# Optimization experiments

Measured on AMD Instinct MI355X. Metric: run time of the kernel, lower is better.

Reference implementation:

```python
import jax, jax.numpy as jnp
import numpy as np

DEPTH, HEADS, DIM_HEAD = 6, 8, 64
B, N, E = 2, 128, 160
NUM_ATOMS, NF = 100, 127
DIM = NF + 1                 # 128, node feature dim fed to transformer
INNER = HEADS * DIM_HEAD     # 512


def setup_inputs() -> dict:
    key = jax.random.key(0)
    ks = iter(jax.random.split(key, 40))
    f32 = jnp.float32
    def w(shape, scale=0.02):
        return jax.random.normal(next(ks), shape, dtype=f32) * scale
    inp = {
        "indices": jax.random.randint(next(ks), (B, N), 0, NUM_ATOMS),
        "coordinates": jax.random.normal(next(ks), (B, N, 3), dtype=f32),
        "bonds": jax.random.randint(next(ks), (E, 2), 0, N),
        "noise_level": jax.random.uniform(next(ks), (1,), dtype=f32),
        "atom_emb": w((NUM_ATOMS, NF), 1.0),
        "ln1_g": jnp.ones((DEPTH, DIM), f32), "ln1_b": jnp.zeros((DEPTH, DIM), f32),
        "Wq": w((DEPTH, DIM, INNER)), "bq": jnp.zeros((DEPTH, INNER), f32),
        "Wkv": w((DEPTH, DIM, 2 * INNER)), "bkv": jnp.zeros((DEPTH, 2 * INNER), f32),
        "We": w((DEPTH, 3, INNER)), "be": jnp.zeros((DEPTH, INNER), f32),
        "Wo": w((DEPTH, INNER, DIM)), "bo": jnp.zeros((DEPTH, DIM), f32),
        "Wg1": w((DEPTH, 3 * DIM, 1)),
        "ln2_g": jnp.ones((DEPTH, DIM), f32), "ln2_b": jnp.zeros((DEPTH, DIM), f32),
        "W1": w((DEPTH, DIM, 4 * DIM)), "b1": jnp.zeros((DEPTH, 4 * DIM), f32),
        "W2": w((DEPTH, 4 * DIM, DIM)), "b2": jnp.zeros((DEPTH, DIM), f32),
        "Wg2": w((DEPTH, 3 * DIM, 1)),
        "Wlin": w((DIM, 1)), "blin": jnp.zeros((1,), f32),
    }
    return inp


def _ln(x, g, b, eps=1e-5):
    m = jnp.mean(x, -1, keepdims=True)
    v = jnp.mean((x - m) ** 2, -1, keepdims=True)
    return (x - m) * jax.lax.rsqrt(v + eps) * g + b


def _gated_residual(x, res, Wg):
    # gate = sigmoid(Linear([x, res, x-res])); out = x*gate + res*(1-gate)
    gate = jax.nn.sigmoid(jnp.concatenate([x, res, x - res], -1) @ Wg)  # (B,N,1)
    return x * gate + res * (1.0 - gate)


def _forward(indices, bonds, coordinates, noise_level, atom_emb,
             ln1_g, ln1_b, Wq, bq, Wkv, bkv, We, be, Wo, bo, Wg1,
             ln2_g, ln2_b, W1, b1, W2, b2, Wg2, Wlin, blin):
    b, n = indices.shape
    # nodes_embedding: atom embedding + noise-level channel
    noise = jnp.broadcast_to(noise_level.reshape(1, 1, 1).astype(coordinates.dtype), (b, n, 1))
    nodes = jnp.concatenate([atom_emb[indices], noise], -1)  # (B,N,DIM)
    # edges_embedding: vectorized scatter of per-bond coordinate differences
    i, j = bonds[:, 0], bonds[:, 1]
    diff = coordinates[:, i] - coordinates[:, j]             # (B,E,3)
    edges = jnp.zeros((b, n, n, 3), coordinates.dtype)
    edges = edges.at[:, i, j].set(diff).at[:, j, i].set(-diff)

    scale = DIM_HEAD ** -0.5
    for l in range(DEPTH):
        # PreNorm + edge-biased attention (mask is all-ones -> no-op)
        xn = _ln(nodes, ln1_g[l], ln1_b[l])
        q = (xn @ Wq[l] + bq[l]).reshape(b, n, HEADS, DIM_HEAD)
        k, v = jnp.split(xn @ Wkv[l] + bkv[l], 2, -1)
        k = k.reshape(b, n, HEADS, DIM_HEAD)
        v = v.reshape(b, n, HEADS, DIM_HEAD)
        e = (edges @ We[l] + be[l]).reshape(b, n, n, HEADS, DIM_HEAD)
        kk = k[:, None] + e                                   # (B,i,j,H,D)
        vv = v[:, None] + e
        sim = jnp.einsum('bihd,bijhd->bijh', q, kk) * scale
        attn = jax.nn.softmax(sim, axis=2)                    # softmax over j
        out = jnp.einsum('bijh,bijhd->bihd', attn, vv).reshape(b, n, INNER)
        out = out @ Wo[l] + bo[l]
        nodes = _gated_residual(out, nodes, Wg1[l])
        # PreNorm + FeedForward (exact GELU, mult=4) + gated residual
        xn = _ln(nodes, ln2_g[l], ln2_b[l])
        ff = jax.nn.gelu(xn @ W1[l] + b1[l], approximate=False) @ W2[l] + b2[l]
        nodes = _gated_residual(ff, nodes, Wg2[l])
    return jnp.sum(nodes @ Wlin + blin)


def reference(indices, coordinates, bonds, noise_level, atom_emb,
              ln1_g, ln1_b, Wq, bq, Wkv, bkv, We, be, Wo, bo, Wg1,
              ln2_g, ln2_b, W1, b1, W2, b2, Wg2, Wlin, blin):
    return _forward(indices, bonds, coordinates, noise_level, atom_emb,
                    ln1_g, ln1_b, Wq, bq, Wkv, bkv, We, be, Wo, bo, Wg1,
                    ln2_g, ln2_b, W1, b1, W2, b2, Wg2, Wlin, blin)
```

## Files before the change

kernel.cpp:

```cpp
#include <hip/hip_runtime.h>
#include <hip/hip_fp16.h>
#include <math.h>

#define DEPTH 6
#define HEADS 8
#define BB    2
#define NN    128
#define EE    160
#define NF    127
#define DIMM  128
#define INNER 512
#define NNODE 256

typedef _Float16 h2f16 __attribute__((ext_vector_type(2)));

#if defined(__has_builtin)
#if __has_builtin(__builtin_amdgcn_fdot2)
#define HAVE_FDOT2 1
#endif
#endif

__device__ __forceinline__ float fdot2f(h2f16 a, h2f16 b, float c) {
#ifdef HAVE_FDOT2
    return __builtin_amdgcn_fdot2(a, b, c, false);
#else
    return c + (float)a.x * (float)b.x + (float)a.y * (float)b.y;
#endif
}

__device__ __forceinline__ void gload16(const void* g, void* l) {
    __builtin_amdgcn_global_load_lds((const __attribute__((address_space(1))) void*)g,
                                     (__attribute__((address_space(3))) void*)l,
                                     16, 0, 0);
}

template <int N>
__device__ __forceinline__ void wait_vm() {
    __builtin_amdgcn_s_waitcnt((0xF << 8) | (7 << 4) | (N & 0xF) | ((N >> 4) << 14));
}
__device__ __forceinline__ void wait_lgkm0() { __builtin_amdgcn_s_waitcnt(0xC07F); }
__device__ __forceinline__ void sbar0() { __builtin_amdgcn_sched_barrier(0); }

__device__ __forceinline__ void stage8s(const char* gslice, int rowstride,
                                        char* ldsslice, int ln) {
#pragma unroll
    for (int i = 0; i < 8; i++)
        gload16(gslice + (size_t)i * rowstride + ln * 16, ldsslice + i * 1024);
}

__device__ __forceinline__ void fma8h(float4& a0, float4& a1, float s, float4 raw) {
    const __half2* hp = (const __half2*)&raw;
    float2 p0 = __half22float2(hp[0]), p1 = __half22float2(hp[1]);
    float2 p2 = __half22float2(hp[2]), p3 = __half22float2(hp[3]);
    a0.x += s * p0.x; a0.y += s * p0.y; a0.z += s * p1.x; a0.w += s * p1.y;
    a1.x += s * p2.x; a1.y += s * p2.y; a1.z += s * p3.x; a1.w += s * p3.y;
}

__device__ __forceinline__ void gemv512_pipe(const float* act, float* wbuf,
                                             float* s_part,
                                             const char* nextA, const char* nextB,
                                             int nextStride, int w, int ln) {
    float4 a0 = {0,0,0,0}, a1 = {0,0,0,0};
    const float4* w4 = (const float4*)wbuf;
    wait_vm<8>();
#pragma unroll
    for (int r = 0; r < 8; r++)
        fma8h(a0, a1, act[w * 16 + r], w4[r * 64 + ln]);
    wait_lgkm0(); sbar0();
    if (nextA) { stage8s(nextA, nextStride, (char*)wbuf, ln); wait_vm<8>(); }
    else       { wait_vm<0>(); }
#pragma unroll
    for (int r = 8; r < 16; r++)
        fma8h(a0, a1, act[w * 16 + r], w4[r * 64 + ln]);
    wait_lgkm0(); sbar0();
    if (nextB) stage8s(nextB, nextStride, (char*)wbuf + 8192, ln);
    ((float4*)(s_part + w * 512))[ln * 2]     = a0;
    ((float4*)(s_part + w * 512))[ln * 2 + 1] = a1;
}

__device__ __forceinline__ void gemv128_pipe(const float* act, float* wbuf,
                                             float* s_part,
                                             const char* nextA, const char* nextB,
                                             int nextStride, int w, int ln) {
    float2 acc = {0, 0};
    wait_vm<8>();
#pragma unroll 8
    for (int r = 0; r < 32; r++) {
        float raw = wbuf[r * 64 + ln];
        float2 p = __half22float2(*(const __half2*)&raw);
        float a = act[w * 64 + r];
        acc.x += a * p.x; acc.y += a * p.y;
    }
    wait_lgkm0(); sbar0();
    if (nextA) { stage8s(nextA, nextStride, (char*)wbuf, ln); wait_vm<8>(); }
    else       { wait_vm<0>(); }
#pragma unroll 8
    for (int r = 32; r < 64; r++) {
        float raw = wbuf[r * 64 + ln];
        float2 p = __half22float2(*(const __half2*)&raw);
        float a = act[w * 64 + r];
        acc.x += a * p.x; acc.y += a * p.y;
    }
    wait_lgkm0(); sbar0();
    if (nextB) stage8s(nextB, nextStride, (char*)wbuf + 8192, ln);
    s_part[w * 128 + ln * 2]     = acc.x;
    s_part[w * 128 + ln * 2 + 1] = acc.y;
}

template <int N>
__device__ __forceinline__ void block_reduce_n(float* vals, float* sbuf) {
#pragma unroll
    for (int off = 32; off > 0; off >>= 1)
#pragma unroll
        for (int q = 0; q < N; q++) vals[q] += __shfl_xor(vals[q], off, 64);
    int wave = threadIdx.x >> 6;
    if ((threadIdx.x & 63) == 0)
#pragma unroll
        for (int q = 0; q < N; q++) sbuf[wave * N + q] = vals[q];
    __syncthreads();
#pragma unroll
    for (int q = 0; q < N; q++) {
        float r = 0.0f;
#pragma unroll
        for (int g = 0; g < 8; g++) r += sbuf[g * N + q];
        vals[q] = r;
    }
    __syncthreads();
}

__device__ __forceinline__ float gelu_exact(float a) {
    return 0.5f * a * (1.0f + erff(a * 0.70710678f));
}


__global__ __launch_bounds__(512) void k_cvt(const float* Wq, const float* Wkv,
                                             const float* Wo, const float* W1,
                                             const float* W2,
                                             __half* hWq, __half* hWkv, __half* hWo,
                                             __half* hW1, __half* hW2,
                                             const float* blin, float* out) {
    if (blockIdx.x == 0 && threadIdx.x == 0) out[0] = 256.0f * blin[0];
    int g = blockIdx.x * 512 + threadIdx.x;
    const float4* src; __half* dst; int off;
    if (g < 98304)       { src = (const float4*)Wq;  dst = hWq;  off = g; }
    else if (g < 294912) { src = (const float4*)Wkv; dst = hWkv; off = g - 98304; }
    else if (g < 393216) { src = (const float4*)Wo;  dst = hWo;  off = g - 294912; }
    else if (g < 491520) { src = (const float4*)W1;  dst = hW1;  off = g - 393216; }
    else                 { src = (const float4*)W2;  dst = hW2;  off = g - 491520; }
    float4 v = src[off];
    __half2* d2 = (__half2*)(dst + (size_t)off * 4);
    d2[0] = __floats2half2_rn(v.x, v.y);
    d2[1] = __floats2half2_rn(v.z, v.w);
}

__global__ __launch_bounds__(512, 1) void k_pre(const int* indices, const float* noise,
                                                const float* atom_emb,
                                                const float* ln1_g, const float* ln1_b,
                                                const __half* hWq, const float* bq,
                                                const __half* hWkv, const float* bkv,
                                                float* nodes, float* qb,
                                                __half* hk, __half* hv) {
    int bn = blockIdx.x;
    int t  = threadIdx.x;
    int d  = t & 127;
    bool own = (t < 128);
    int w = t >> 6, ln = t & 63;
    __shared__ float arena[32768];
    __shared__ float s_xn[128];
    __shared__ float s_red[48];
    __shared__ float s_part[4096];
    char*  lslice = (char*)arena + w * 16384;
    float* wbuf   = arena + w * 4096;

    const char* WqL  = (const char*)hWq;
    const char* WkvL = (const char*)hWkv;
    stage8s(WqL + w * 16384, 1024, lslice, ln);
    stage8s(WqL + w * 16384 + 8192, 1024, lslice + 8192, ln);

    float nd = 0.0f;
    if (own) {
        int idx = indices[bn];
        nd = (d < NF) ? atom_emb[idx * NF + d] : noise[0];
        nodes[bn * DIMM + d] = nd;
    }
    float vals[2] = {own ? nd : 0.0f, own ? nd * nd : 0.0f};
    block_reduce_n<2>(vals, s_red);
    float m   = vals[0] * (1.0f / 128.0f);
    float var = vals[1] * (1.0f / 128.0f) - m * m;
    if (own) s_xn[d] = (nd - m) * rsqrtf(var + 1e-5f) * ln1_g[d] + ln1_b[d];
    __syncthreads();

    gemv512_pipe(s_xn, wbuf, s_part,
                 WkvL + (size_t)(w * 16) * 2048,
                 WkvL + (size_t)(w * 16 + 8) * 2048, 2048, w, ln);
    __syncthreads();
    {
        float q = bq[t];
#pragma unroll
        for (int g = 0; g < 8; g++) q += s_part[g * 512 + t];
        qb[(size_t)bn * INNER + t] = q;
    }
    __syncthreads();

    gemv512_pipe(s_xn, wbuf, s_part,
                 WkvL + (size_t)(w * 16) * 2048 + 1024,
                 WkvL + (size_t)(w * 16 + 8) * 2048 + 1024, 2048, w, ln);
    __syncthreads();
    {
        float k = bkv[t];
#pragma unroll
        for (int g = 0; g < 8; g++) k += s_part[g * 512 + t];
        hk[(size_t)bn * INNER + t] = __float2half(k);
    }
    __syncthreads();

    gemv512_pipe(s_xn, wbuf, s_part, nullptr, nullptr, 0, w, ln);
    __syncthreads();
    {
        float v = bkv[INNER + t];
#pragma unroll
        for (int g = 0; g < 8; g++) v += s_part[g * 512 + t];
        hv[(size_t)bn * INNER + t] = __float2half(v);
    }
}

__global__ __launch_bounds__(512, 1) void k_layer(int l,
        const float* coords, const int* bonds,
        const float* We, const float* be,
        float* qb, const __half* hkin, const __half* hvin,
        __half* hkout, __half* hvout,
        const __half* hWo, const float* bo, const float* Wg1,
        const float* ln2_g, const float* ln2_b,
        const __half* hW1, const float* b1,
        const __half* hW2, const float* b2,
        const float* Wg2,
        const float* ln1_g, const float* ln1_b,
        const __half* hWq, const float* bq,
        const __half* hWkv, const float* bkv,
        float* nodes, const float* Wlin, float* out) {
    int bn = blockIdx.x;
    int b = bn >> 7, i = bn & 127;
    int t = threadIdx.x;
    int d = t & 127;
    bool own = (t < 128);
    int w = t >> 6, ln = t & 63;

    __shared__ float arena[32768];
    __shared__ float scoord[384];
    __shared__ float sedge[384];
    __shared__ int   sadj[128];
    __shared__ float s_l[64];
    __shared__ float s_ao[512];
    __shared__ float s_h[512];
    __shared__ float s_xn[128];
    __shared__ float s_red[48];
    __shared__ float s_part[4096];
    float* s_o = s_part;
    char*  lslice = (char*)arena + w * 16384;
    float* wbuf   = arena + w * 4096;

    const char* WoL  = (const char*)(hWo + (size_t)l * INNER * DIMM);
    const char* W1L  = (const char*)(hW1 + (size_t)l * DIMM * 4 * DIMM);
    const char* W2L  = (const char*)(hW2 + (size_t)l * 4 * DIMM * DIMM);
    const char* WqL  = (const char*)(hWq + (size_t)(l + 1) * DIMM * INNER);
    const char* WkvL = (const char*)(hWkv + (size_t)(l + 1) * DIMM * 2 * INNER);

    stage8s(WoL + w * 16384, 1024, lslice, ln);
    stage8s(WoL + w * 16384 + 8192, 1024, lslice + 8192, ln);

    const float4* qR4 = (const float4*)(qb + (size_t)bn * INNER);
    const float4* WeR = (const float4*)(We + (size_t)l * 3 * INNER);
    float4 qa  = qR4[ln * 2],        qz  = qR4[ln * 2 + 1];
    float4 w0a = WeR[ln * 2],        w0z = WeR[ln * 2 + 1];
    float4 w1a = WeR[128 + ln * 2],  w1z = WeR[129 + ln * 2];
    float4 w2a = WeR[256 + ln * 2],  w2z = WeR[257 + ln * 2];
    float4 bea = ((const float4*)(be + (size_t)l * INNER))[ln * 2];
    float4 bez = ((const float4*)(be + (size_t)l * INNER))[ln * 2 + 1];
    float res = own ? nodes[bn * DIMM + d] : 0.0f;
    h2f16 qh0 = {(_Float16)qa.x, (_Float16)qa.y};
    h2f16 qh1 = {(_Float16)qa.z, (_Float16)qa.w};
    h2f16 qh2 = {(_Float16)qz.x, (_Float16)qz.y};
    h2f16 qh3 = {(_Float16)qz.z, (_Float16)qz.w};
    float c = qa.x * bea.x + qa.y * bea.y + qa.z * bea.z + qa.w * bea.w
            + qz.x * bez.x + qz.y * bez.y + qz.z * bez.z + qz.w * bez.w;
    c += __shfl_xor(c, 1, 64); c += __shfl_xor(c, 2, 64); c += __shfl_xor(c, 4, 64);

    if (t < 3 * NN) scoord[t] = coords[b * 3 * NN + t];
    if (t < NN) sadj[t] = 0;
    __syncthreads();
    if (t < EE) {
        int e0 = bonds[2 * t], e1 = bonds[2 * t + 1];
        if (e0 == i) sadj[e1] = 1;
        if (e1 == i) sadj[e0] = 1;
    }
    __syncthreads();
    if (t < NN) {
        int j = t;
        float msk = sadj[j] ? 1.0f : 0.0f;
        sedge[3 * j + 0] = msk * (scoord[3 * i + 0] - scoord[3 * j + 0]);
        sedge[3 * j + 1] = msk * (scoord[3 * i + 1] - scoord[3 * j + 1]);
        sedge[3 * j + 2] = msk * (scoord[3 * i + 2] - scoord[3 * j + 2]);
    }
    __syncthreads();

    const float4* kR = (const float4*)(hkin + (size_t)b * NN * INNER);
    const float4* vR = (const float4*)(hvin + (size_t)b * NN * INNER);
    float l_run = 0.0f, S_nb = 0.0f;
    float4 o0 = {0, 0, 0, 0}, o1 = {0, 0, 0, 0};
    int j0 = w * 16;
#pragma unroll
    for (int base = 0; base < 16; base += 4) {
        float4 kraw[4], vraw[4];
#pragma unroll
        for (int p = 0; p < 4; p++) {
            int j = j0 + base + p;
            kraw[p] = kR[j * 64 + ln];
            vraw[p] = vR[j * 64 + ln];
        }
#pragma unroll
        for (int p = 0; p < 4; p++) {
            int j = j0 + base + p;
            const h2f16* kh = (const h2f16*)&kraw[p];
            float s = fdot2f(qh0, kh[0],
                      fdot2f(qh1, kh[1],
                      fdot2f(qh2, kh[2],
                      fdot2f(qh3, kh[3], 0.0f))));
            bool bonded = (sadj[j] != 0);
            float4 e0, e1;
            if (bonded) {
                float ex = sedge[3 * j], ey = sedge[3 * j + 1], ez = sedge[3 * j + 2];
                e0.x = bea.x + ex * w0a.x + ey * w1a.x + ez * w2a.x;
                e0.y = bea.y + ex * w0a.y + ey * w1a.y + ez * w2a.y;
                e0.z = bea.z + ex * w0a.z + ey * w1a.z + ez * w2a.z;
                e0.w = bea.w + ex * w0a.w + ey * w1a.w + ez * w2a.w;
                e1.x = bez.x + ex * w0z.x + ey * w1z.x + ez * w2z.x;
                e1.y = bez.y + ex * w0z.y + ey * w1z.y + ez * w2z.y;
                e1.z = bez.z + ex * w0z.z + ey * w1z.z + ez * w2z.z;
                e1.w = bez.w + ex * w0z.w + ey * w1z.w + ez * w2z.w;
                s += qa.x * e0.x + qa.y * e0.y + qa.z * e0.z + qa.w * e0.w
                   + qz.x * e1.x + qz.y * e1.y + qz.z * e1.z + qz.w * e1.w;
            }
            s += __shfl_xor(s, 1, 64);
            s += __shfl_xor(s, 2, 64);
            s += __shfl_xor(s, 4, 64);
            if (!bonded) s += c;
            float pp = __expf(s * 0.125f);
            l_run += pp;
            const __half2* vh = (const __half2*)&vraw[p];
            float2 v0 = __half22float2(vh[0]), v1 = __half22float2(vh[1]);
            float2 v2 = __half22float2(vh[2]), v3 = __half22float2(vh[3]);
            o0.x += pp * v0.x; o0.y += pp * v0.y; o0.z += pp * v1.x; o0.w += pp * v1.y;
            o1.x += pp * v2.x; o1.y += pp * v2.y; o1.z += pp * v3.x; o1.w += pp * v3.y;
            if (bonded) {
                o0.x += pp * e0.x; o0.y += pp * e0.y; o0.z += pp * e0.z; o0.w += pp * e0.w;
                o1.x += pp * e1.x; o1.y += pp * e1.y; o1.z += pp * e1.z; o1.w += pp * e1.w;
            } else S_nb += pp;
        }
    }
    o0.x += S_nb * bea.x; o0.y += S_nb * bea.y; o0.z += S_nb * bea.z; o0.w += S_nb * bea.w;
    o1.x += S_nb * bez.x; o1.y += S_nb * bez.y; o1.z += S_nb * bez.z; o1.w += S_nb * bez.w;
    ((float4*)(s_o + w * 512))[ln * 2]     = o0;
    ((float4*)(s_o + w * 512))[ln * 2 + 1] = o1;
    if ((ln & 7) == 0) s_l[w * 8 + (ln >> 3)] = l_run;
    __syncthreads();
    {
        float o = 0.0f;
#pragma unroll
        for (int g = 0; g < 8; g++) o += s_o[g * 512 + t];
        int h = t >> 6;
        float lsum = 0.0f;
#pragma unroll
        for (int g = 0; g < 8; g++) lsum += s_l[g * 8 + h];
        s_ao[t] = o / lsum;
    }
    __syncthreads();

    gemv128_pipe(s_ao, wbuf, s_part,
                 W1L + w * 16384, W1L + w * 16384 + 8192, 1024, w, ln);
    __syncthreads();
    float x = 0.0f;
    if (own) {
        x = bo[l * DIMM + d];
#pragma unroll
        for (int g = 0; g < 8; g++) x += s_part[g * 128 + d];
    }

    const float* Wg1_l = Wg1 + l * 3 * DIMM;
    float n1;
    {
        float tex = own ? (x * Wg1_l[d] + res * Wg1_l[DIMM + d]
                           + (x - res) * Wg1_l[2 * DIMM + d]) : 0.0f;
        float vals[6] = {tex,
                         own ? x : 0.0f, own ? x * x : 0.0f,
                         own ? x * res : 0.0f,
                         own ? res : 0.0f, own ? res * res : 0.0f};
        block_reduce_n<6>(vals, s_red);
        float g1 = 1.0f / (1.0f + __expf(-vals[0]));
        float sn  = g1 * vals[1] + (1.0f - g1) * vals[4];
        float sn2 = g1 * g1 * vals[2] + 2.0f * g1 * (1.0f - g1) * vals[3]
                  + (1.0f - g1) * (1.0f - g1) * vals[5];
        float m   = sn * (1.0f / 128.0f);
        float var = sn2 * (1.0f / 128.0f) - m * m;
        n1 = x * g1 + res * (1.0f - g1);
        if (own) s_xn[d] = (n1 - m) * rsqrtf(var + 1e-5f) * ln2_g[l * DIMM + d]
                         + ln2_b[l * DIMM + d];
    }
    __syncthreads();

    gemv512_pipe(s_xn, wbuf, s_part,
                 W2L + w * 16384, W2L + w * 16384 + 8192, 1024, w, ln);
    __syncthreads();
    {
        float a = b1[l * 4 * DIMM + t];
#pragma unroll
        for (int g = 0; g < 8; g++) a += s_part[g * 512 + t];
        s_h[t] = gelu_exact(a);
    }
    __syncthreads();

    gemv128_pipe(s_h, wbuf, s_part,
                 (l < DEPTH - 1) ? WqL + w * 16384 : nullptr,
                 (l < DEPTH - 1) ? WqL + w * 16384 + 8192 : nullptr, 1024, w, ln);
    __syncthreads();
    float y = 0.0f;
    if (own) {
        y = b2[l * DIMM + d];
#pragma unroll
        for (int g = 0; g < 8; g++) y += s_part[g * 128 + d];
    }

    const float* Wg2_l = Wg2 + l * 3 * DIMM;
    if (l < DEPTH - 1) {
        float tex = own ? (y * Wg2_l[d] + n1 * Wg2_l[DIMM + d]
                           + (y - n1) * Wg2_l[2 * DIMM + d]) : 0.0f;
        float vals[6] = {tex,
                         own ? y : 0.0f, own ? y * y : 0.0f,
                         own ? y * n1 : 0.0f,
                         own ? n1 : 0.0f, own ? n1 * n1 : 0.0f};
        block_reduce_n<6>(vals, s_red);
        float g2 = 1.0f / (1.0f + __expf(-vals[0]));
        float sn  = g2 * vals[1] + (1.0f - g2) * vals[4];
        float sn2 = g2 * g2 * vals[2] + 2.0f * g2 * (1.0f - g2) * vals[3]
                  + (1.0f - g2) * (1.0f - g2) * vals[5];
        float m   = sn * (1.0f / 128.0f);
        float var = sn2 * (1.0f / 128.0f) - m * m;
        float n2 = y * g2 + n1 * (1.0f - g2);
        if (own) {
            nodes[bn * DIMM + d] = n2;
            s_xn[d] = (n2 - m) * rsqrtf(var + 1e-5f) * ln1_g[(l + 1) * DIMM + d]
                    + ln1_b[(l + 1) * DIMM + d];
        }
        __syncthreads();

        gemv512_pipe(s_xn, wbuf, s_part,
                     WkvL + (size_t)(w * 16) * 2048,
                     WkvL + (size_t)(w * 16 + 8) * 2048, 2048, w, ln);
        __syncthreads();
        {
            float q = bq[(l + 1) * INNER + t];
#pragma unroll
            for (int g = 0; g < 8; g++) q += s_part[g * 512 + t];
            qb[(size_t)bn * INNER + t] = q;
        }
        __syncthreads();

        gemv512_pipe(s_xn, wbuf, s_part,
                     WkvL + (size_t)(w * 16) * 2048 + 1024,
                     WkvL + (size_t)(w * 16 + 8) * 2048 + 1024, 2048, w, ln);
        __syncthreads();
        {
            float k = bkv[(l + 1) * 2 * INNER + t];
#pragma unroll
            for (int g = 0; g < 8; g++) k += s_part[g * 512 + t];
            hkout[(size_t)bn * INNER + t] = __float2half(k);
        }
        __syncthreads();

        gemv512_pipe(s_xn, wbuf, s_part, nullptr, nullptr, 0, w, ln);
        __syncthreads();
        {
            float v = bkv[(l + 1) * 2 * INNER + INNER + t];
#pragma unroll
            for (int g = 0; g < 8; g++) v += s_part[g * 512 + t];
            hvout[(size_t)bn * INNER + t] = __float2half(v);
        }
    } else {
        float wl = own ? Wlin[d] : 0.0f;
        float tex = own ? (y * Wg2_l[d] + n1 * Wg2_l[DIMM + d]
                           + (y - n1) * Wg2_l[2 * DIMM + d]) : 0.0f;
        float vals[3] = {tex, y * wl, n1 * wl};
        block_reduce_n<3>(vals, s_red);
        float g2 = 1.0f / (1.0f + __expf(-vals[0]));
        float tot = g2 * vals[1] + (1.0f - g2) * vals[2];
        if (t == 0) atomicAdd(out, tot);
    }
}

extern "C" void kernel_launch(void* const* d_in, const int* in_sizes, int n_in,
                              void* d_out, int out_size, void* d_ws, size_t ws_size,
                              hipStream_t stream) {
    const int*   indices = (const int*)d_in[0];
    const float* coords  = (const float*)d_in[1];
    const int*   bonds   = (const int*)d_in[2];
    const float* noise   = (const float*)d_in[3];
    const float* atom_emb= (const float*)d_in[4];
    const float* ln1_g   = (const float*)d_in[5];
    const float* ln1_b   = (const float*)d_in[6];
    const float* Wq      = (const float*)d_in[7];
    const float* bq      = (const float*)d_in[8];
    const float* Wkv     = (const float*)d_in[9];
    const float* bkv     = (const float*)d_in[10];
    const float* We      = (const float*)d_in[11];
    const float* be      = (const float*)d_in[12];
    const float* Wo      = (const float*)d_in[13];
    const float* bo      = (const float*)d_in[14];
    const float* Wg1     = (const float*)d_in[15];
    const float* ln2_g   = (const float*)d_in[16];
    const float* ln2_b   = (const float*)d_in[17];
    const float* W1      = (const float*)d_in[18];
    const float* b1      = (const float*)d_in[19];
    const float* W2      = (const float*)d_in[20];
    const float* b2      = (const float*)d_in[21];
    const float* Wg2     = (const float*)d_in[22];
    const float* Wlin    = (const float*)d_in[23];
    const float* blin    = (const float*)d_in[24];

    float*  ws    = (float*)d_ws;
    float*  nodes = ws;
    float*  qb    = nodes + NNODE * DIMM;
    __half* hkb   = (__half*)(qb + NNODE * INNER);
    __half* hvb   = hkb + 2 * NNODE * INNER;
    __half* hWq   = hvb + 2 * NNODE * INNER;
    __half* hWkv  = hWq + DEPTH * DIMM * INNER;
    __half* hWo   = hWkv + DEPTH * DIMM * 2 * INNER;
    __half* hW1   = hWo + DEPTH * INNER * DIMM;
    __half* hW2   = hW1 + DEPTH * DIMM * 4 * DIMM;

    k_cvt<<<1152, 512, 0, stream>>>(Wq, Wkv, Wo, W1, W2, hWq, hWkv, hWo, hW1, hW2,
                                    blin, (float*)d_out);
    k_pre<<<NNODE, 512, 0, stream>>>(indices, noise, atom_emb, ln1_g, ln1_b,
                                     hWq, bq, hWkv, bkv, nodes, qb, hkb, hvb);
    for (int l = 0; l < DEPTH; l++) {
        const __half* hkin = hkb + (size_t)(l & 1) * NNODE * INNER;
        const __half* hvin = hvb + (size_t)(l & 1) * NNODE * INNER;
        __half* hkout = hkb + (size_t)((l + 1) & 1) * NNODE * INNER;
        __half* hvout = hvb + (size_t)((l + 1) & 1) * NNODE * INNER;
        k_layer<<<NNODE, 512, 0, stream>>>(l, coords, bonds, We, be,
                                           qb, hkin, hvin, hkout, hvout,
                                           hWo, bo, Wg1, ln2_g, ln2_b, hW1, b1, hW2, b2,
                                           Wg2, ln1_g, ln1_b, hWq, bq, hWkv, bkv,
                                           nodes, Wlin, (float*)d_out);
    }
}
```

Measured before the change: 259.6 us.

## Double block size to 1024 threads and re-split GEMV and attention work

Launches k_pre and k_layer with 1024 threads (16 waves) instead of 512. Each wave now handles half the rows of the attention key range and half the column range of every GEMV, with new staging helpers that load half-width weight slices. Partial sums are reduced across 16 waves, and the attention output reduction runs in two passes through shared memory. The aim is more latency hiding and memory parallelism per block, at the cost of extra barriers, a larger reduction and higher register pressure under the 1024-thread launch bound.

```diff
diff --git a/kernel.cpp b/kernel.cpp
--- a/kernel.cpp
+++ b/kernel.cpp
@@ -41,68 +41,81 @@
 __device__ __forceinline__ void wait_lgkm0() { __builtin_amdgcn_s_waitcnt(0xC07F); }
 __device__ __forceinline__ void sbar0() { __builtin_amdgcn_sched_barrier(0); }
 
-__device__ __forceinline__ void stage8s(const char* gslice, int rowstride,
-                                        char* ldsslice, int ln) {
-#pragma unroll
-    for (int i = 0; i < 8; i++)
-        gload16(gslice + (size_t)i * rowstride + ln * 16, ldsslice + i * 1024);
-}
-
-__device__ __forceinline__ void fma8h(float4& a0, float4& a1, float s, float4 raw) {
-    const __half2* hp = (const __half2*)&raw;
-    float2 p0 = __half22float2(hp[0]), p1 = __half22float2(hp[1]);
-    float2 p2 = __half22float2(hp[2]), p3 = __half22float2(hp[3]);
-    a0.x += s * p0.x; a0.y += s * p0.y; a0.z += s * p1.x; a0.w += s * p1.y;
-    a1.x += s * p2.x; a1.y += s * p2.y; a1.z += s * p3.x; a1.w += s * p3.y;
-}
-
-__device__ __forceinline__ void gemv512_pipe(const float* act, float* wbuf,
-                                             float* s_part,
-                                             const char* nextA, const char* nextB,
-                                             int nextStride, int w, int ln) {
-    float4 a0 = {0,0,0,0}, a1 = {0,0,0,0};
-    const float4* w4 = (const float4*)wbuf;
-    wait_vm<8>();
-#pragma unroll
-    for (int r = 0; r < 8; r++)
-        fma8h(a0, a1, act[w * 16 + r], w4[r * 64 + ln]);
+__device__ __forceinline__ void stage4c(const char* g, char* lds, int ln) {
+#pragma unroll
+    for (int i = 0; i < 4; i++)
+        gload16(g + i * 1024 + ln * 16, lds + i * 1024);
+}
+__device__ __forceinline__ void stage4h(const char* g, int rs, char* lds, int ln) {
+#pragma unroll
+    for (int i = 0; i < 4; i++)
+        gload16(g + (size_t)(2 * i + (ln >> 5)) * rs + (ln & 31) * 16, lds + i * 1024);
+}
+
+
+template <int NK>
+__device__ __forceinline__ void gemv512x(const float* act, float* wbuf,
+                                         float* s_part, int w, int ln,
+                                         const char* nextA, const char* nextB,
+                                         int nextRS) {
+    int kg = w >> 1;
+    float4 acc = {0, 0, 0, 0};
+    const float2* w2 = (const float2*)wbuf;
+    wait_vm<4>();
+#pragma unroll
+    for (int r = 0; r < 8; r++) {
+        float2 raw = w2[r * 64 + ln];
+        const __half2* hp = (const __half2*)&raw;
+        float2 p0 = __half22float2(hp[0]), p1 = __half22float2(hp[1]);
+        float a = act[kg * 16 + r];
+        acc.x += a * p0.x; acc.y += a * p0.y; acc.z += a * p1.x; acc.w += a * p1.y;
+    }
     wait_lgkm0(); sbar0();
-    if (nextA) { stage8s(nextA, nextStride, (char*)wbuf, ln); wait_vm<8>(); }
-    else       { wait_vm<0>(); }
-#pragma unroll
-    for (int r = 8; r < 16; r++)
-        fma8h(a0, a1, act[w * 16 + r], w4[r * 64 + ln]);
+    if (NK == 1)      { stage4c(nextA, (char*)wbuf, ln);         wait_vm<4>(); }
+    else if (NK == 2) { stage4h(nextA, nextRS, (char*)wbuf, ln); wait_vm<4>(); }
+    else              { wait_vm<0>(); }
+#pragma unroll
+    for (int r = 8; r < 16; r++) {
+        float2 raw = w2[r * 64 + ln];
+        const __half2* hp = (const __half2*)&raw;
+        float2 p0 = __half22float2(hp[0]), p1 = __half22float2(hp[1]);
+        float a = act[kg * 16 + r];
+        acc.x += a * p0.x; acc.y += a * p0.y; acc.z += a * p1.x; acc.w += a * p1.y;
+    }
     wait_lgkm0(); sbar0();
-    if (nextB) stage8s(nextB, nextStride, (char*)wbuf + 8192, ln);
-    ((float4*)(s_part + w * 512))[ln * 2]     = a0;
-    ((float4*)(s_part + w * 512))[ln * 2 + 1] = a1;
-}
-
-__device__ __forceinline__ void gemv128_pipe(const float* act, float* wbuf,
-                                             float* s_part,
-                                             const char* nextA, const char* nextB,
-                                             int nextStride, int w, int ln) {
+    if (NK == 1)      stage4c(nextB, (char*)wbuf + 4096, ln);
+    else if (NK == 2) stage4h(nextB, nextRS, (char*)wbuf + 4096, ln);
+    ((float4*)(s_part + w * 256))[ln] = acc;
+}
+
+template <int NK>
+__device__ __forceinline__ void gemv128x(const float* act, float* wbuf,
+                                         float* s_part, int w, int ln,
+                                         const char* nextA, const char* nextB,
+                                         int nextRS) {
     float2 acc = {0, 0};
-    wait_vm<8>();
+    wait_vm<4>();
 #pragma unroll 8
-    for (int r = 0; r < 32; r++) {
+    for (int r = 0; r < 16; r++) {
         float raw = wbuf[r * 64 + ln];
         float2 p = __half22float2(*(const __half2*)&raw);
-        float a = act[w * 64 + r];
+        float a = act[w * 32 + r];
         acc.x += a * p.x; acc.y += a * p.y;
     }
     wait_lgkm0(); sbar0();
-    if (nextA) { stage8s(nextA, nextStride, (char*)wbuf, ln); wait_vm<8>(); }
-    else       { wait_vm<0>(); }
+    if (NK == 1)      { stage4c(nextA, (char*)wbuf, ln);         wait_vm<4>(); }
+    else if (NK == 2) { stage4h(nextA, nextRS, (char*)wbuf, ln); wait_vm<4>(); }
+    else              { wait_vm<0>(); }
 #pragma unroll 8
-    for (int r = 32; r < 64; r++) {
+    for (int r = 16; r < 32; r++) {
         float raw = wbuf[r * 64 + ln];
         float2 p = __half22float2(*(const __half2*)&raw);
-        float a = act[w * 64 + r];
+        float a = act[w * 32 + r];
         acc.x += a * p.x; acc.y += a * p.y;
     }
     wait_lgkm0(); sbar0();
-    if (nextB) stage8s(nextB, nextStride, (char*)wbuf + 8192, ln);
+    if (NK == 1)      stage4c(nextB, (char*)wbuf + 4096, ln);
+    else if (NK == 2) stage4h(nextB, nextRS, (char*)wbuf + 4096, ln);
     s_part[w * 128 + ln * 2]     = acc.x;
     s_part[w * 128 + ln * 2 + 1] = acc.y;
 }
@@ -122,7 +135,7 @@
     for (int q = 0; q < N; q++) {
         float r = 0.0f;
 #pragma unroll
-        for (int g = 0; g < 8; g++) r += sbuf[g * N + q];
+        for (int g = 0; g < 16; g++) r += sbuf[g * N + q];
         vals[q] = r;
     }
     __syncthreads();
@@ -153,29 +166,30 @@
     d2[1] = __floats2half2_rn(v.z, v.w);
 }
 
-__global__ __launch_bounds__(512, 1) void k_pre(const int* indices, const float* noise,
-                                                const float* atom_emb,
-                                                const float* ln1_g, const float* ln1_b,
-                                                const __half* hWq, const float* bq,
-                                                const __half* hWkv, const float* bkv,
-                                                float* nodes, float* qb,
-                                                __half* hk, __half* hv) {
+__global__ __launch_bounds__(1024, 4) void k_pre(const int* indices, const float* noise,
+                                                 const float* atom_emb,
+                                                 const float* ln1_g, const float* ln1_b,
+                                                 const __half* hWq, const float* bq,
+                                                 const __half* hWkv, const float* bkv,
+                                                 float* nodes, float* qb,
+                                                 __half* hk, __half* hv) {
     int bn = blockIdx.x;
     int t  = threadIdx.x;
     int d  = t & 127;
     bool own = (t < 128);
     int w = t >> 6, ln = t & 63;
+    int kg = w >> 1, ch = w & 1;
     __shared__ float arena[32768];
     __shared__ float s_xn[128];
-    __shared__ float s_red[48];
+    __shared__ float s_red[96];
     __shared__ float s_part[4096];
-    char*  lslice = (char*)arena + w * 16384;
-    float* wbuf   = arena + w * 4096;
+    float* wbuf = arena + w * 2048;
 
     const char* WqL  = (const char*)hWq;
     const char* WkvL = (const char*)hWkv;
-    stage8s(WqL + w * 16384, 1024, lslice, ln);
-    stage8s(WqL + w * 16384 + 8192, 1024, lslice + 8192, ln);
+
+    stage4h(WqL + (size_t)(kg * 16) * 1024 + ch * 512, 1024, (char*)wbuf, ln);
+    stage4h(WqL + (size_t)(kg * 16 + 8) * 1024 + ch * 512, 1024, (char*)wbuf + 4096, ln);
 
     float nd = 0.0f;
     if (own) {
@@ -190,41 +204,44 @@
     if (own) s_xn[d] = (nd - m) * rsqrtf(var + 1e-5f) * ln1_g[d] + ln1_b[d];
     __syncthreads();
 
-    gemv512_pipe(s_xn, wbuf, s_part,
-                 WkvL + (size_t)(w * 16) * 2048,
-                 WkvL + (size_t)(w * 16 + 8) * 2048, 2048, w, ln);
-    __syncthreads();
-    {
+    gemv512x<2>(s_xn, wbuf, s_part, w, ln,
+                WkvL + (size_t)(kg * 16) * 2048 + ch * 512,
+                WkvL + (size_t)(kg * 16 + 8) * 2048 + ch * 512, 2048);
+    __syncthreads();
+    if (t < 512) {
+        int lc = t & 255, cch = t >> 8;
         float q = bq[t];
 #pragma unroll
-        for (int g = 0; g < 8; g++) q += s_part[g * 512 + t];
+        for (int g = 0; g < 8; g++) q += s_part[(g * 2 + cch) * 256 + lc];
         qb[(size_t)bn * INNER + t] = q;
     }
     __syncthreads();
 
-    gemv512_pipe(s_xn, wbuf, s_part,
-                 WkvL + (size_t)(w * 16) * 2048 + 1024,
-                 WkvL + (size_t)(w * 16 + 8) * 2048 + 1024, 2048, w, ln);
-    __syncthreads();
-    {
+    gemv512x<2>(s_xn, wbuf, s_part, w, ln,
+                WkvL + (size_t)(kg * 16) * 2048 + 1024 + ch * 512,
+                WkvL + (size_t)(kg * 16 + 8) * 2048 + 1024 + ch * 512, 2048);
+    __syncthreads();
+    if (t < 512) {
+        int lc = t & 255, cch = t >> 8;
         float k = bkv[t];
 #pragma unroll
-        for (int g = 0; g < 8; g++) k += s_part[g * 512 + t];
+        for (int g = 0; g < 8; g++) k += s_part[(g * 2 + cch) * 256 + lc];
         hk[(size_t)bn * INNER + t] = __float2half(k);
     }
     __syncthreads();
 
-    gemv512_pipe(s_xn, wbuf, s_part, nullptr, nullptr, 0, w, ln);
-    __syncthreads();
-    {
+    gemv512x<0>(s_xn, wbuf, s_part, w, ln, nullptr, nullptr, 0);
+    __syncthreads();
+    if (t < 512) {
+        int lc = t & 255, cch = t >> 8;
         float v = bkv[INNER + t];
 #pragma unroll
-        for (int g = 0; g < 8; g++) v += s_part[g * 512 + t];
+        for (int g = 0; g < 8; g++) v += s_part[(g * 2 + cch) * 256 + lc];
         hv[(size_t)bn * INNER + t] = __float2half(v);
     }
 }
 
-__global__ __launch_bounds__(512, 1) void k_layer(int l,
+__global__ __launch_bounds__(1024, 4) void k_layer(int l,
         const float* coords, const int* bonds,
         const float* We, const float* be,
         float* qb, const __half* hkin, const __half* hvin,
@@ -244,20 +261,19 @@
     int d = t & 127;
     bool own = (t < 128);
     int w = t >> 6, ln = t & 63;
+    int kg = w >> 1, ch = w & 1;
 
     __shared__ float arena[32768];
     __shared__ float scoord[384];
     __shared__ float sedge[384];
     __shared__ int   sadj[128];
-    __shared__ float s_l[64];
+    __shared__ float s_l[128];
     __shared__ float s_ao[512];
     __shared__ float s_h[512];
     __shared__ float s_xn[128];
-    __shared__ float s_red[48];
+    __shared__ float s_red[96];
     __shared__ float s_part[4096];
-    float* s_o = s_part;
-    char*  lslice = (char*)arena + w * 16384;
-    float* wbuf   = arena + w * 4096;
+    float* wbuf = arena + w * 2048;
 
     const char* WoL  = (const char*)(hWo + (size_t)l * INNER * DIMM);
     const char* W1L  = (const char*)(hW1 + (size_t)l * DIMM * 4 * DIMM);
@@ -265,8 +281,8 @@
     const char* WqL  = (const char*)(hWq + (size_t)(l + 1) * DIMM * INNER);
     const char* WkvL = (const char*)(hWkv + (size_t)(l + 1) * DIMM * 2 * INNER);
 
-    stage8s(WoL + w * 16384, 1024, lslice, ln);
-    stage8s(WoL + w * 16384 + 8192, 1024, lslice + 8192, ln);
+    stage4c(WoL + w * 8192, (char*)wbuf, ln);
+    stage4c(WoL + w * 8192 + 4096, (char*)wbuf + 4096, ln);
 
     const float4* qR4 = (const float4*)(qb + (size_t)bn * INNER);
     const float4* WeR = (const float4*)(We + (size_t)l * 3 * INNER);
@@ -307,9 +323,9 @@
     const float4* vR = (const float4*)(hvin + (size_t)b * NN * INNER);
     float l_run = 0.0f, S_nb = 0.0f;
     float4 o0 = {0, 0, 0, 0}, o1 = {0, 0, 0, 0};
-    int j0 = w * 16;
-#pragma unroll
-    for (int base = 0; base < 16; base += 4) {
+    int j0 = w * 8;
+#pragma unroll
+    for (int base = 0; base < 8; base += 4) {
         float4 kraw[4], vraw[4];
 #pragma unroll
         for (int p = 0; p < 4; p++) {
@@ -359,30 +375,44 @@
     }
     o0.x += S_nb * bea.x; o0.y += S_nb * bea.y; o0.z += S_nb * bea.z; o0.w += S_nb * bea.w;
     o1.x += S_nb * bez.x; o1.y += S_nb * bez.y; o1.z += S_nb * bez.z; o1.w += S_nb * bez.w;
-    ((float4*)(s_o + w * 512))[ln * 2]     = o0;
-    ((float4*)(s_o + w * 512))[ln * 2 + 1] = o1;
     if ((ln & 7) == 0) s_l[w * 8 + (ln >> 3)] = l_run;
-    __syncthreads();
-    {
-        float o = 0.0f;
-#pragma unroll
-        for (int g = 0; g < 8; g++) o += s_o[g * 512 + t];
+
+    if (w < 8) {
+        ((float4*)(s_part + w * 512))[ln * 2]     = o0;
+        ((float4*)(s_part + w * 512))[ln * 2 + 1] = o1;
+    }
+    __syncthreads();
+    float oacc = 0.0f;
+    if (t < 512) {
+#pragma unroll
+        for (int g = 0; g < 8; g++) oacc += s_part[g * 512 + t];
+    }
+    __syncthreads();
+    if (w >= 8) {
+        ((float4*)(s_part + (w - 8) * 512))[ln * 2]     = o0;
+        ((float4*)(s_part + (w - 8) * 512))[ln * 2 + 1] = o1;
+    }
+    __syncthreads();
+    if (t < 512) {
+#pragma unroll
+        for (int g = 0; g < 8; g++) oacc += s_part[g * 512 + t];
         int h = t >> 6;
         float lsum = 0.0f;
 #pragma unroll
-        for (int g = 0; g < 8; g++) lsum += s_l[g * 8 + h];
-        s_ao[t] = o / lsum;
-    }
-    __syncthreads();
-
-    gemv128_pipe(s_ao, wbuf, s_part,
-                 W1L + w * 16384, W1L + w * 16384 + 8192, 1024, w, ln);
+        for (int g = 0; g < 16; g++) lsum += s_l[g * 8 + h];
+        s_ao[t] = oacc / lsum;
+    }
+    __syncthreads();
+
+    gemv128x<2>(s_ao, wbuf, s_part, w, ln,
+                W1L + (size_t)(kg * 16) * 1024 + ch * 512,
+                W1L + (size_t)(kg * 16 + 8) * 1024 + ch * 512, 1024);
     __syncthreads();
     float x = 0.0f;
     if (own) {
         x = bo[l * DIMM + d];
 #pragma unroll
-        for (int g = 0; g < 8; g++) x += s_part[g * 128 + d];
+        for (int g = 0; g < 16; g++) x += s_part[g * 128 + d];
     }
 
     const float* Wg1_l = Wg1 + l * 3 * DIMM;
@@ -407,26 +437,30 @@
     }
     __syncthreads();
 
-    gemv512_pipe(s_xn, wbuf, s_part,
-                 W2L + w * 16384, W2L + w * 16384 + 8192, 1024, w, ln);
-    __syncthreads();
-    {
+    gemv512x<1>(s_xn, wbuf, s_part, w, ln,
+                W2L + w * 8192, W2L + w * 8192 + 4096, 0);
+    __syncthreads();
+    if (t < 512) {
+        int lc = t & 255, cch = t >> 8;
         float a = b1[l * 4 * DIMM + t];
 #pragma unroll
-        for (int g = 0; g < 8; g++) a += s_part[g * 512 + t];
+        for (int g = 0; g < 8; g++) a += s_part[(g * 2 + cch) * 256 + lc];
         s_h[t] = gelu_exact(a);
     }
     __syncthreads();
 
-    gemv128_pipe(s_h, wbuf, s_part,
-                 (l < DEPTH - 1) ? WqL + w * 16384 : nullptr,
-                 (l < DEPTH - 1) ? WqL + w * 16384 + 8192 : nullptr, 1024, w, ln);
+    if (l < DEPTH - 1)
+        gemv128x<2>(s_h, wbuf, s_part, w, ln,
+                    WqL + (size_t)(kg * 16) * 1024 + ch * 512,
+                    WqL + (size_t)(kg * 16 + 8) * 1024 + ch * 512, 1024);
+    else
+        gemv128x<0>(s_h, wbuf, s_part, w, ln, nullptr, nullptr, 0);
     __syncthreads();
     float y = 0.0f;
     if (own) {
         y = b2[l * DIMM + d];
 #pragma unroll
-        for (int g = 0; g < 8; g++) y += s_part[g * 128 + d];
+        for (int g = 0; g < 16; g++) y += s_part[g * 128 + d];
     }
 
     const float* Wg2_l = Wg2 + l * 3 * DIMM;
@@ -452,36 +486,39 @@
         }
         __syncthreads();
 
-        gemv512_pipe(s_xn, wbuf, s_part,
-                     WkvL + (size_t)(w * 16) * 2048,
-                     WkvL + (size_t)(w * 16 + 8) * 2048, 2048, w, ln);
+        gemv512x<2>(s_xn, wbuf, s_part, w, ln,
+                    WkvL + (size_t)(kg * 16) * 2048 + ch * 512,
+                    WkvL + (size_t)(kg * 16 + 8) * 2048 + ch * 512, 2048);
         __syncthreads();
-        {
+        if (t < 512) {
+            int lc = t & 255, cch = t >> 8;
             float q = bq[(l + 1) * INNER + t];
 #pragma unroll
-            for (int g = 0; g < 8; g++) q += s_part[g * 512 + t];
+            for (int g = 0; g < 8; g++) q += s_part[(g * 2 + cch) * 256 + lc];
             qb[(size_t)bn * INNER + t] = q;
         }
         __syncthreads();
 
-        gemv512_pipe(s_xn, wbuf, s_part,
-                     WkvL + (size_t)(w * 16) * 2048 + 1024,
-                     WkvL + (size_t)(w * 16 + 8) * 2048 + 1024, 2048, w, ln);
+        gemv512x<2>(s_xn, wbuf, s_part, w, ln,
+                    WkvL + (size_t)(kg * 16) * 2048 + 1024 + ch * 512,
+                    WkvL + (size_t)(kg * 16 + 8) * 2048 + 1024 + ch * 512, 2048);
         __syncthreads();
-        {
+        if (t < 512) {
+            int lc = t & 255, cch = t >> 8;
             float k = bkv[(l + 1) * 2 * INNER + t];
 #pragma unroll
-            for (int g = 0; g < 8; g++) k += s_part[g * 512 + t];
+            for (int g = 0; g < 8; g++) k += s_part[(g * 2 + cch) * 256 + lc];
             hkout[(size_t)bn * INNER + t] = __float2half(k);
         }
         __syncthreads();
 
-        gemv512_pipe(s_xn, wbuf, s_part, nullptr, nullptr, 0, w, ln);
+        gemv512x<0>(s_xn, wbuf, s_part, w, ln, nullptr, nullptr, 0);
         __syncthreads();
-        {
+        if (t < 512) {
+            int lc = t & 255, cch = t >> 8;
             float v = bkv[(l + 1) * 2 * INNER + INNER + t];
 #pragma unroll
-            for (int g = 0; g < 8; g++) v += s_part[g * 512 + t];
+            for (int g = 0; g < 8; g++) v += s_part[(g * 2 + cch) * 256 + lc];
             hvout[(size_t)bn * INNER + t] = __float2half(v);
         }
     } else {
@@ -538,17 +575,17 @@
 
     k_cvt<<<1152, 512, 0, stream>>>(Wq, Wkv, Wo, W1, W2, hWq, hWkv, hWo, hW1, hW2,
                                     blin, (float*)d_out);
-    k_pre<<<NNODE, 512, 0, stream>>>(indices, noise, atom_emb, ln1_g, ln1_b,
-                                     hWq, bq, hWkv, bkv, nodes, qb, hkb, hvb);
+    k_pre<<<NNODE, 1024, 0, stream>>>(indices, noise, atom_emb, ln1_g, ln1_b,
+                                      hWq, bq, hWkv, bkv, nodes, qb, hkb, hvb);
     for (int l = 0; l < DEPTH; l++) {
         const __half* hkin = hkb + (size_t)(l & 1) * NNODE * INNER;
         const __half* hvin = hvb + (size_t)(l & 1) * NNODE * INNER;
         __half* hkout = hkb + (size_t)((l + 1) & 1) * NNODE * INNER;
         __half* hvout = hvb + (size_t)((l + 1) & 1) * NNODE * INNER;
-        k_layer<<<NNODE, 512, 0, stream>>>(l, coords, bonds, We, be,
-                                           qb, hkin, hvin, hkout, hvout,
-                                           hWo, bo, Wg1, ln2_g, ln2_b, hW1, b1, hW2, b2,
-                                           Wg2, ln1_g, ln1_b, hWq, bq, hWkv, bkv,
-                                           nodes, Wlin, (float*)d_out);
-    }
-}
+        k_layer<<<NNODE, 1024, 0, stream>>>(l, coords, bonds, We, be,
+                                            qb, hkin, hvin, hkout, hvout,
+                                            hWo, bo, Wg1, ln2_g, ln2_b, hW1, b1, hW2, b2,
+                                            Wg2, ln1_g, ln1_b, hWq, bq, hWkv, bkv,
+                                            nodes, Wlin, (float*)d_out);
+    }
+}
```

Measured after the change: 288.7 us. +11.2%, slower.
